# Performance work log

Hardware: AMD Instinct MI355X
Metric: run time of the kernel (lower is better)

Reference implementation:

```python
import jax, jax.numpy as jnp
import numpy as np

B, S, D = 2, 4096, 768
H = 12
HD = D // H  # 64
INNER = 4 * D
EPS = 1e-5


def setup_inputs() -> dict:
    key = jax.random.key(0)
    ks = jax.random.split(key, 12)
    sd = 0.02
    # causal additive mask (GPT-2 style): 0 where allowed, -1e9 where masked
    causal = jnp.tril(jnp.ones((S, S), dtype=bool))
    attention_mask = jnp.where(causal, 0.0, -1e9).astype(jnp.float32)[None, None]
    return {
        "hidden_states": jax.random.normal(ks[0], (B, S, D), dtype=jnp.float32),
        "attention_mask": attention_mask,
        "ln1_g": jnp.ones((D,), jnp.float32),
        "ln1_b": jnp.zeros((D,), jnp.float32),
        "w_attn": jax.random.normal(ks[1], (D, 3 * D), jnp.float32) * sd,
        "b_attn": jnp.zeros((3 * D,), jnp.float32),
        "w_cproj": jax.random.normal(ks[2], (D, D), jnp.float32) * sd,
        "b_cproj": jnp.zeros((D,), jnp.float32),
        "ln2_g": jnp.ones((D,), jnp.float32),
        "ln2_b": jnp.zeros((D,), jnp.float32),
        "w_fc": jax.random.normal(ks[3], (D, INNER), jnp.float32) * sd,
        "b_fc": jnp.zeros((INNER,), jnp.float32),
        "w_fc_proj": jax.random.normal(ks[4], (INNER, D), jnp.float32) * sd,
        "b_fc_proj": jnp.zeros((D,), jnp.float32),
    }


def _layernorm(x, g, b):
    mu = jnp.mean(x, axis=-1, keepdims=True)
    var = jnp.mean(jnp.square(x - mu), axis=-1, keepdims=True)
    return (x - mu) * jax.lax.rsqrt(var + EPS) * g + b


def reference(hidden_states, attention_mask, ln1_g, ln1_b, w_attn, b_attn,
              w_cproj, b_cproj, ln2_g, ln2_b, w_fc, b_fc, w_fc_proj, b_fc_proj):
    residual = hidden_states
    x = _layernorm(hidden_states, ln1_g, ln1_b)
    # qkv projection
    qkv = x @ w_attn + b_attn                       # [B,S,3D]
    q, k, v = jnp.split(qkv, 3, axis=-1)
    q = q.reshape(B, S, H, HD).transpose(0, 2, 1, 3)  # [B,H,S,HD]
    k = k.reshape(B, S, H, HD).transpose(0, 2, 1, 3)
    v = v.reshape(B, S, H, HD).transpose(0, 2, 1, 3)
    scale = HD ** -0.5
    scores = jnp.einsum('bhqd,bhkd->bhqk', q, k) * scale + attention_mask
    attn = jax.nn.softmax(scores, axis=-1)
    ctx = jnp.einsum('bhqk,bhkd->bhqd', attn, v)    # [B,H,S,HD]
    ctx = ctx.transpose(0, 2, 1, 3).reshape(B, S, D)
    attn_out = ctx @ w_cproj + b_cproj
    h = attn_out + residual
    residual = h
    y = _layernorm(h, ln2_g, ln2_b)
    y = jax.nn.gelu(y @ w_fc + b_fc, approximate=False)  # nn.GELU default = exact
    y = y @ w_fc_proj + b_fc_proj
    return y + residual
```

## Files before the change

kernel.cpp:

```cpp
#include <hip/hip_runtime.h>
#include <hip/hip_bf16.h>


#define S_     4096
#define D_     768
#define H_     12
#define HD_    64
#define NB_    2
#define M_     (NB_*S_)
#define QKV_   (3*D_)
#define INNER_ 3072

typedef unsigned short u16;
typedef __attribute__((ext_vector_type(4))) float f32x4;
typedef __attribute__((ext_vector_type(8))) short s16x8;

__device__ __forceinline__ float bf2f(u16 h) {
    union { unsigned int u; float f; } c; c.u = ((unsigned int)h) << 16; return c.f;
}
__device__ __forceinline__ u16 f2bf(float f) {
    union { float f; unsigned int u; } c; c.f = f;
    return (u16)((c.u + 0x7fffu + ((c.u >> 16) & 1u)) >> 16);
}
__device__ __forceinline__ void storev(u16* p, float v) { *p = f2bf(v); }
__device__ __forceinline__ void storev(float* p, float v) { *p = v; }

__device__ __forceinline__ float fexp2(float x) {
#if __has_builtin(__builtin_amdgcn_exp2f)
    return __builtin_amdgcn_exp2f(x);
#else
    return __expf(x * 0.69314718056f);
#endif
}
__device__ __forceinline__ unsigned int packbf(float a, float b) {
    union { __hip_bfloat162 h; unsigned int u; } c;
    c.h = __float22bfloat162_rn(float2{a, b});
    return c.u;
}

__device__ __forceinline__ void gload_lds16(const u16* g, u16* l) {
    __builtin_amdgcn_global_load_lds((const __attribute__((address_space(1))) void*)g,
                                     (__attribute__((address_space(3))) void*)l, 16, 0, 0);
}

template <typename IT, bool PERM>
__global__ __launch_bounds__(256) void transpose_kernel(const IT* __restrict__ in,
                                                        u16* __restrict__ out,
                                                        int ld_in, int ld_out) {
    __shared__ u16 tile[32][33];
    const int c0 = blockIdx.x * 32, r0 = blockIdx.y * 32;
    const int tx = threadIdx.x & 31, ty = threadIdx.x >> 5;
#pragma unroll
    for (int i = 0; i < 32; i += 8) {
        IT v = in[(size_t)(r0 + ty + i) * ld_in + c0 + tx];
        u16 bv;
        if constexpr (sizeof(IT) == 4) bv = f2bf((float)v); else bv = (u16)v;
        tile[ty + i][tx] = bv;
    }
    __syncthreads();
    int oc = r0 + tx;
    if constexpr (PERM) oc = (oc & ~63) | (((oc & 15) << 2) | ((oc >> 4) & 3));
#pragma unroll
    for (int i = 0; i < 32; i += 8)
        out[(size_t)(c0 + ty + i) * ld_out + oc] = tile[tx][ty + i];
}

__global__ __launch_bounds__(256) void ln_row(const float* __restrict__ x, const float* __restrict__ g,
                                              const float* __restrict__ bb, u16* __restrict__ y,
                                              unsigned int* ctr) {
    const int row = blockIdx.x;
    const int tid = threadIdx.x;
    if (ctr && row == 0 && tid == 0) *ctr = 0u;
    const float* xr = x + (size_t)row * D_;
    float v0 = xr[tid], v1 = xr[tid + 256], v2 = xr[tid + 512];
    float s = v0 + v1 + v2, s2 = v0 * v0 + v1 * v1 + v2 * v2;
#pragma unroll
    for (int d = 32; d >= 1; d >>= 1) { s += __shfl_xor(s, d, 64); s2 += __shfl_xor(s2, d, 64); }
    __shared__ float red[8];
    const int wave = tid >> 6, lane = tid & 63;
    if (lane == 0) { red[wave] = s; red[4 + wave] = s2; }
    __syncthreads();
    s = red[0] + red[1] + red[2] + red[3];
    s2 = red[4] + red[5] + red[6] + red[7];
    const float mu = s * (1.0f / D_);
    const float var = s2 * (1.0f / D_) - mu * mu;
    const float rstd = rsqrtf(var + 1e-5f);
    u16* yr = y + (size_t)row * D_;
    yr[tid]       = f2bf((v0 - mu) * rstd * g[tid]       + bb[tid]);
    yr[tid + 256] = f2bf((v1 - mu) * rstd * g[tid + 256] + bb[tid + 256]);
    yr[tid + 512] = f2bf((v2 - mu) * rstd * g[tid + 512] + bb[tid + 512]);
}

template <int EPI, typename OT>
__global__ __launch_bounds__(256) void gemm_bt(const u16* __restrict__ A, const u16* __restrict__ Bt,
                                               const float* __restrict__ bias, const float* res,
                                               OT* C, int M, int N, int K) {
    __shared__ u16 As[128 * 32];
    __shared__ u16 Bs[128 * 32];
    const int tid = threadIdx.x;
    const int wave = tid >> 6, lane = tid & 63;
    const int m0 = blockIdx.y << 7, n0 = blockIdx.x << 7;
    const int fr = lane & 15, quad = lane >> 4;

    const int srow = wave * 16 + (lane >> 2);
    const int scol = (lane & 3) * 8;
    const u16* ag0 = A + (size_t)(m0 + srow) * K + scol;
    const u16* ag1 = ag0 + (size_t)64 * K;
    const u16* bg0 = Bt + (size_t)(n0 + srow) * K + scol;
    const u16* bg1 = bg0 + (size_t)64 * K;
    u16* al0 = As + wave * 512;
    u16* al1 = As + 2048 + wave * 512;
    u16* bl0 = Bs + wave * 512;
    u16* bl1 = Bs + 2048 + wave * 512;

    const f32x4 fz = {0.f, 0.f, 0.f, 0.f};
    f32x4 acc[4][4];
#pragma unroll
    for (int i = 0; i < 4; i++)
#pragma unroll
        for (int j = 0; j < 4; j++) acc[i][j] = fz;

    const int wm = wave & 1, wn = wave >> 1;
    const u16* a_rd = As + (wm * 64 + fr) * 32 + quad * 8;
    const u16* b_rd = Bs + (wn * 64 + fr) * 32 + quad * 8;

    for (int k0 = 0; k0 < K; k0 += 32) {
        gload_lds16(ag0 + k0, al0);
        gload_lds16(ag1 + k0, al1);
        gload_lds16(bg0 + k0, bl0);
        gload_lds16(bg1 + k0, bl1);
        __syncthreads();
        s16x8 af[4], bfr[4];
#pragma unroll
        for (int t = 0; t < 4; t++) {
            af[t]  = *(const s16x8*)(a_rd + t * 16 * 32);
            bfr[t] = *(const s16x8*)(b_rd + t * 16 * 32);
        }
#pragma unroll
        for (int mt = 0; mt < 4; mt++)
#pragma unroll
            for (int nt = 0; nt < 4; nt++)
                acc[mt][nt] = __builtin_amdgcn_mfma_f32_16x16x32_bf16(af[mt], bfr[nt], acc[mt][nt], 0, 0, 0);
        __syncthreads();
    }

    const int crow0 = m0 + wm * 64 + quad * 4;
    const int ccol0 = n0 + wn * 64 + fr;
#pragma unroll
    for (int nt = 0; nt < 4; nt++) {
        const int col = ccol0 + nt * 16;
        const float bv = bias[col];
#pragma unroll
        for (int mt = 0; mt < 4; mt++) {
#pragma unroll
            for (int r = 0; r < 4; r++) {
                const int row = crow0 + mt * 16 + r;
                float v = acc[mt][nt][r] + bv;
                if constexpr (EPI == 1) v = 0.5f * v * (1.0f + erff(v * 0.70710678118654752f));
                if constexpr (EPI == 2) v += res[(size_t)row * N + col];
                storev(&C[(size_t)row * N + col], v);
            }
        }
    }
}

template <int EPI, typename OT>
__global__ __launch_bounds__(256) void gemm_bt64(const u16* __restrict__ A, const u16* __restrict__ Bt,
                                                 const float* __restrict__ bias, const float* res,
                                                 OT* C, int M, int N, int K) {
    __shared__ u16 As[128 * 32];
    __shared__ u16 Bs[64 * 32];
    const int tid = threadIdx.x;
    const int wave = tid >> 6, lane = tid & 63;
    const int m0 = blockIdx.y << 7, n0 = blockIdx.x << 6;
    const int fr = lane & 15, quad = lane >> 4;

    const int srow = wave * 16 + (lane >> 2);
    const int scol = (lane & 3) * 8;
    const u16* ag0 = A + (size_t)(m0 + srow) * K + scol;
    const u16* ag1 = ag0 + (size_t)64 * K;
    const u16* bg0 = Bt + (size_t)(n0 + srow) * K + scol;
    u16* al0 = As + wave * 512;
    u16* al1 = As + 2048 + wave * 512;
    u16* bl0 = Bs + wave * 512;

    const f32x4 fz = {0.f, 0.f, 0.f, 0.f};
    f32x4 acc[2][4];
#pragma unroll
    for (int i = 0; i < 2; i++)
#pragma unroll
        for (int j = 0; j < 4; j++) acc[i][j] = fz;

    const u16* a_rd = As + (wave * 32 + fr) * 32 + quad * 8;
    const u16* b_rd = Bs + fr * 32 + quad * 8;

    for (int k0 = 0; k0 < K; k0 += 32) {
        gload_lds16(ag0 + k0, al0);
        gload_lds16(ag1 + k0, al1);
        gload_lds16(bg0 + k0, bl0);
        __syncthreads();
        s16x8 af[2], bfr[4];
#pragma unroll
        for (int t = 0; t < 2; t++) af[t] = *(const s16x8*)(a_rd + t * 16 * 32);
#pragma unroll
        for (int t = 0; t < 4; t++) bfr[t] = *(const s16x8*)(b_rd + t * 16 * 32);
#pragma unroll
        for (int mt = 0; mt < 2; mt++)
#pragma unroll
            for (int nt = 0; nt < 4; nt++)
                acc[mt][nt] = __builtin_amdgcn_mfma_f32_16x16x32_bf16(af[mt], bfr[nt], acc[mt][nt], 0, 0, 0);
        __syncthreads();
    }

    const int crow0 = m0 + wave * 32 + quad * 4;
    const int ccol0 = n0 + fr;
#pragma unroll
    for (int nt = 0; nt < 4; nt++) {
        const int col = ccol0 + nt * 16;
        const float bv = bias[col];
#pragma unroll
        for (int mt = 0; mt < 2; mt++) {
#pragma unroll
            for (int r = 0; r < 4; r++) {
                const int row = crow0 + mt * 16 + r;
                float v = acc[mt][nt][r] + bv;
                if constexpr (EPI == 1) v = 0.5f * v * (1.0f + erff(v * 0.70710678118654752f));
                if constexpr (EPI == 2) v += res[(size_t)row * N + col];
                storev(&C[(size_t)row * N + col], v);
            }
        }
    }
}

#define SCALE_  0.1803368801111f
#define PST_    72
#define NITEMS_ (32 * H_ * NB_)
#define NWORK_  512
__global__ __launch_bounds__(256, 2) void flash_attn(const u16* __restrict__ qkv, const u16* __restrict__ vt,
                                                     u16* __restrict__ ctx, unsigned int* __restrict__ ctr) {
    const int tid = threadIdx.x;
    const int wave = tid >> 6, lane = tid & 63;
    const int fr = lane & 15, quad = lane >> 4;

    __shared__ u16 Ks[2][64 * 64];
    __shared__ u16 Vs[2][64 * 64];
    __shared__ u16 Ps4[4][32 * PST_];
    __shared__ int item_sh;
    u16* Ps = Ps4[wave];

    const int rsub = lane >> 3;
    const int schunk = ((lane & 7) ^ rsub) << 3;
    u16* KlS0 = &Ks[0][(wave << 4) * 64];
    u16* VlS0 = &Vs[0][(wave << 4) * 64];

    const f32x4 fz = {0.f, 0.f, 0.f, 0.f};
    s16x8 ones;
#pragma unroll
    for (int j = 0; j < 8; j++) ones[j] = (short)0x3F80;

    for (;;) {
        if (tid == 0) item_sh = (int)atomicAdd(ctr, 1u);
        __syncthreads();
        const int item = item_sh;
        if (item >= NITEMS_) return;

        const int strip = 31 - item / (H_ * NB_);
        const int hb = item % (H_ * NB_);
        const int h = hb % H_, b = hb / H_;
        const int q0 = strip << 7;
        const int qwv = q0 + (wave << 5);

        const u16* Qg  = qkv + ((size_t)b * S_ + qwv) * QKV_ + h * HD_;
        const u16* Kg  = qkv + (size_t)b * S_ * QKV_ + D_ + h * HD_;
        const u16* Vtg = vt + ((size_t)b * D_ + h * HD_) * S_;
        const u16* KgS = Kg + (size_t)((wave << 4) + rsub) * QKV_ + schunk;
        const u16* VgS = Vtg + (size_t)((wave << 4) + rsub) * S_ + schunk;

        s16x8 qf[2][2];
#pragma unroll
        for (int mt = 0; mt < 2; mt++)
#pragma unroll
            for (int kk = 0; kk < 2; kk++)
                qf[mt][kk] = *(const s16x8*)(Qg + (size_t)(mt * 16 + fr) * QKV_ + kk * 32 + quad * 8);

        f32x4 o[2][4];
        f32x4 ls[2];
#pragma unroll
        for (int mt = 0; mt < 2; mt++) {
            ls[mt] = fz;
#pragma unroll
            for (int nt = 0; nt < 4; nt++) o[mt][nt] = fz;
        }

        const int ntw = (strip << 1) + 2;

        gload_lds16(KgS, KlS0);
        gload_lds16(KgS + (size_t)8 * QKV_, KlS0 + 512);
        gload_lds16(VgS, VlS0);
        gload_lds16(VgS + (size_t)8 * S_, VlS0 + 512);
        asm volatile("s_waitcnt vmcnt(0)" ::: "memory");
        __syncthreads();

        int cur = 0;
        for (int t = 0; t < ntw; t++) {
            const int k0 = t << 6;

            if (t + 1 < ntw) {
                const int nb = cur ^ 1;
                const u16* kg = KgS + (size_t)((t + 1) << 6) * QKV_;
                const u16* vg = VgS + ((t + 1) << 6);
                u16* kl = KlS0 + nb * (64 * 64);
                u16* vl = VlS0 + nb * (64 * 64);
                gload_lds16(kg, kl);
                gload_lds16(kg + (size_t)8 * QKV_, kl + 512);
                gload_lds16(vg, vl);
                gload_lds16(vg + (size_t)8 * S_, vl + 512);
            }

            if (k0 <= qwv + 31) {
                const u16* kb = Ks[cur];
                const u16* vb = Vs[cur];

                s16x8 kc[2][4];
#pragma unroll
                for (int kk = 0; kk < 2; kk++)
#pragma unroll
                    for (int nt = 0; nt < 4; nt++) {
                        const int row = nt * 16 + fr;
                        const int sl = ((kk * 4 + quad) ^ (fr & 7)) << 3;
                        kc[kk][nt] = *(const s16x8*)(kb + row * 64 + sl);
                    }

                f32x4 sc[2][4];
#pragma unroll
                for (int mt = 0; mt < 2; mt++)
#pragma unroll
                    for (int nt = 0; nt < 4; nt++) sc[mt][nt] = fz;
#pragma unroll
                for (int kk = 0; kk < 2; kk++)
#pragma unroll
                    for (int mt = 0; mt < 2; mt++)
#pragma unroll
                        for (int nt = 0; nt < 4; nt++)
                            sc[mt][nt] = __builtin_amdgcn_mfma_f32_16x16x32_bf16(qf[mt][kk], kc[kk][nt], sc[mt][nt], 0, 0, 0);

                const bool fast = (k0 + 63 <= qwv);
#pragma unroll
                for (int mt = 0; mt < 2; mt++) {
#pragma unroll
                    for (int r = 0; r < 4; r++) {
                        float s0 = sc[mt][0][r] * SCALE_;
                        float s1 = sc[mt][1][r] * SCALE_;
                        float s2 = sc[mt][2][r] * SCALE_;
                        float s3 = sc[mt][3][r] * SCALE_;
                        if (!fast) {
                            const int lim = (qwv + mt * 16 + quad * 4 + r) - k0;
                            if (fr      > lim) s0 = -1e30f;
                            if (fr + 16 > lim) s1 = -1e30f;
                            if (fr + 32 > lim) s2 = -1e30f;
                            if (fr + 48 > lim) s3 = -1e30f;
                        }
                        s0 = fexp2(s0); s1 = fexp2(s1); s2 = fexp2(s2); s3 = fexp2(s3);
                        const int prow = mt * 16 + quad * 4 + r;
                        *(uint2*)(Ps + prow * PST_ + fr * 4) = make_uint2(packbf(s0, s1), packbf(s2, s3));
                    }
                }

                s16x8 vf[2][4];
#pragma unroll
                for (int kk = 0; kk < 2; kk++)
#pragma unroll
                    for (int nt = 0; nt < 4; nt++) {
                        const int row = nt * 16 + fr;
                        const int sl = ((kk * 4 + quad) ^ (fr & 7)) << 3;
                        vf[kk][nt] = *(const s16x8*)(vb + row * 64 + sl);
                    }

                s16x8 pf[2][2];
#pragma unroll
                for (int mt = 0; mt < 2; mt++)
#pragma unroll
                    for (int kk = 0; kk < 2; kk++)
                        pf[mt][kk] = *(const s16x8*)(Ps + (mt * 16 + fr) * PST_ + kk * 32 + quad * 8);

#pragma unroll
                for (int mt = 0; mt < 2; mt++) {
                    ls[mt] = __builtin_amdgcn_mfma_f32_16x16x32_bf16(pf[mt][0], ones, ls[mt], 0, 0, 0);
                    ls[mt] = __builtin_amdgcn_mfma_f32_16x16x32_bf16(pf[mt][1], ones, ls[mt], 0, 0, 0);
                }
#pragma unroll
                for (int kk = 0; kk < 2; kk++)
#pragma unroll
                    for (int mt = 0; mt < 2; mt++)
#pragma unroll
                        for (int nt = 0; nt < 4; nt++)
                            o[mt][nt] = __builtin_amdgcn_mfma_f32_16x16x32_bf16(pf[mt][kk], vf[kk][nt], o[mt][nt], 0, 0, 0);
            }

            asm volatile("s_waitcnt vmcnt(0)" ::: "memory");
            __syncthreads();
            cur ^= 1;
        }

#pragma unroll
        for (int mt = 0; mt < 2; mt++) {
#pragma unroll
            for (int r = 0; r < 4; r++) {
                const int grow = qwv + mt * 16 + quad * 4 + r;
                const float inv = 1.0f / ls[mt][r];
                u16* crow = ctx + ((size_t)b * S_ + grow) * D_ + h * HD_ + fr;
#pragma unroll
                for (int nt = 0; nt < 4; nt++)
                    crow[nt * 16] = f2bf(o[mt][nt][r] * inv);
            }
        }
    }
}

extern "C" void kernel_launch(void* const* d_in, const int* in_sizes, int n_in,
                              void* d_out, int out_size, void* d_ws, size_t ws_size,
                              hipStream_t stream) {
    const float* hid    = (const float*)d_in[0];
    const float* ln1g   = (const float*)d_in[2];
    const float* ln1b   = (const float*)d_in[3];
    const float* w_attn = (const float*)d_in[4];
    const float* b_attn = (const float*)d_in[5];
    const float* w_cp   = (const float*)d_in[6];
    const float* b_cp   = (const float*)d_in[7];
    const float* ln2g   = (const float*)d_in[8];
    const float* ln2b   = (const float*)d_in[9];
    const float* w_fc   = (const float*)d_in[10];
    const float* b_fc   = (const float*)d_in[11];
    const float* w_fp   = (const float*)d_in[12];
    const float* b_fp   = (const float*)d_in[13];
    float* dout = (float*)d_out;

    unsigned int* ctr = (unsigned int*)d_out;

    u16* ws = (u16*)d_ws;
    u16* wTa  = ws; ws += (size_t)QKV_ * D_;
    u16* wTc  = ws; ws += (size_t)D_ * D_;
    u16* wTf  = ws; ws += (size_t)INNER_ * D_;
    u16* wTp  = ws; ws += (size_t)D_ * INNER_;
    u16* xln  = ws; ws += (size_t)M_ * D_;
    u16* qkvb = ws; ws += (size_t)M_ * QKV_;
    u16* vtb  = ws; ws += (size_t)NB_ * D_ * S_;
    u16* ctxb = xln;
    u16* yln  = xln;
    u16* act  = qkvb;

    dim3 blk(256);
    transpose_kernel<float, false><<<dim3(QKV_ / 32, D_ / 32), blk, 0, stream>>>(w_attn, wTa, QKV_, D_);
    transpose_kernel<float, false><<<dim3(D_ / 32, D_ / 32), blk, 0, stream>>>(w_cp, wTc, D_, D_);
    transpose_kernel<float, false><<<dim3(INNER_ / 32, D_ / 32), blk, 0, stream>>>(w_fc, wTf, INNER_, D_);
    transpose_kernel<float, false><<<dim3(D_ / 32, INNER_ / 32), blk, 0, stream>>>(w_fp, wTp, D_, INNER_);

    ln_row<<<M_, blk, 0, stream>>>(hid, ln1g, ln1b, xln, ctr);
    gemm_bt<0, u16><<<dim3(QKV_ / 128, M_ / 128), blk, 0, stream>>>(xln, wTa, b_attn, nullptr, qkvb, M_, QKV_, D_);

    transpose_kernel<u16, true><<<dim3(D_ / 32, S_ / 32), blk, 0, stream>>>(qkvb + 2 * D_, vtb, QKV_, S_);
    transpose_kernel<u16, true><<<dim3(D_ / 32, S_ / 32), blk, 0, stream>>>(qkvb + (size_t)S_ * QKV_ + 2 * D_,
                                                                            vtb + (size_t)D_ * S_, QKV_, S_);
    flash_attn<<<dim3(NWORK_), blk, 0, stream>>>(qkvb, vtb, ctxb, ctr);

    gemm_bt64<2, float><<<dim3(D_ / 64, M_ / 128), blk, 0, stream>>>(ctxb, wTc, b_cp, hid, dout, M_, D_, D_);
    ln_row<<<M_, blk, 0, stream>>>(dout, ln2g, ln2b, yln, nullptr);
    gemm_bt<1, u16><<<dim3(INNER_ / 128, M_ / 128), blk, 0, stream>>>(yln, wTf, b_fc, nullptr, act, M_, INNER_, D_);
    gemm_bt64<2, float><<<dim3(D_ / 64, M_ / 128), blk, 0, stream>>>(act, wTp, b_fp, dout, dout, M_, D_, INNER_);
}
```

Before: 527.9 us.

## Triple-buffer GEMM and attention LDS loads with prefetch depth two

Moves both GEMM kernels from single-buffered LDS staging, which waited on each load before computing, to a three-stage ring that prefetches two K-steps ahead with partial vmcnt waits. The attention kernel goes from double to triple buffering of K/V tiles. It also raises wave priority around the MFMA blocks with s_setprio. The cost is three times the GEMM LDS footprint and more attention LDS, which may reduce occupancy.

Measured after the change: 527.8 us. Within noise of the previous version (-0.0%).

```diff
diff --git a/kernel.cpp b/kernel.cpp
--- a/kernel.cpp
+++ b/kernel.cpp
@@ -42,6 +42,8 @@
     __builtin_amdgcn_global_load_lds((const __attribute__((address_space(1))) void*)g,
                                      (__attribute__((address_space(3))) void*)l, 16, 0, 0);
 }
+
+#define WAITVM(N) asm volatile("s_waitcnt vmcnt(" #N ")" ::: "memory")
 
 template <typename IT, bool PERM>
 __global__ __launch_bounds__(256) void transpose_kernel(const IT* __restrict__ in,
@@ -95,8 +97,8 @@
 __global__ __launch_bounds__(256) void gemm_bt(const u16* __restrict__ A, const u16* __restrict__ Bt,
                                                const float* __restrict__ bias, const float* res,
                                                OT* C, int M, int N, int K) {
-    __shared__ u16 As[128 * 32];
-    __shared__ u16 Bs[128 * 32];
+    __shared__ u16 As[3][128 * 32];
+    __shared__ u16 Bs[3][128 * 32];
     const int tid = threadIdx.x;
     const int wave = tid >> 6, lane = tid & 63;
     const int m0 = blockIdx.y << 7, n0 = blockIdx.x << 7;
@@ -108,10 +110,13 @@
     const u16* ag1 = ag0 + (size_t)64 * K;
     const u16* bg0 = Bt + (size_t)(n0 + srow) * K + scol;
     const u16* bg1 = bg0 + (size_t)64 * K;
-    u16* al0 = As + wave * 512;
-    u16* al1 = As + 2048 + wave * 512;
-    u16* bl0 = Bs + wave * 512;
-    u16* bl1 = Bs + 2048 + wave * 512;
+
+    auto STAGE = [&](int k0, int b) {
+        gload_lds16(ag0 + k0, &As[b][wave * 512]);
+        gload_lds16(ag1 + k0, &As[b][2048 + wave * 512]);
+        gload_lds16(bg0 + k0, &Bs[b][wave * 512]);
+        gload_lds16(bg1 + k0, &Bs[b][2048 + wave * 512]);
+    };
 
     const f32x4 fz = {0.f, 0.f, 0.f, 0.f};
     f32x4 acc[4][4];
@@ -121,26 +126,30 @@
         for (int j = 0; j < 4; j++) acc[i][j] = fz;
 
     const int wm = wave & 1, wn = wave >> 1;
-    const u16* a_rd = As + (wm * 64 + fr) * 32 + quad * 8;
-    const u16* b_rd = Bs + (wn * 64 + fr) * 32 + quad * 8;
-
-    for (int k0 = 0; k0 < K; k0 += 32) {
-        gload_lds16(ag0 + k0, al0);
-        gload_lds16(ag1 + k0, al1);
-        gload_lds16(bg0 + k0, bl0);
-        gload_lds16(bg1 + k0, bl1);
-        __syncthreads();
+    const int a_off = (wm * 64 + fr) * 32 + quad * 8;
+    const int b_off = (wn * 64 + fr) * 32 + quad * 8;
+
+    const int nsteps = K >> 5;
+    STAGE(0, 0);
+    if (nsteps > 1) { STAGE(32, 1); WAITVM(4); } else { WAITVM(0); }
+    __syncthreads();
+
+    for (int t = 0; t < nsteps; t++) {
+        if (t + 2 < nsteps) STAGE((t + 2) << 5, (t + 2) % 3);
+        const u16* a_rd = &As[t % 3][a_off];
+        const u16* b_rd = &Bs[t % 3][b_off];
         s16x8 af[4], bfr[4];
 #pragma unroll
-        for (int t = 0; t < 4; t++) {
-            af[t]  = *(const s16x8*)(a_rd + t * 16 * 32);
-            bfr[t] = *(const s16x8*)(b_rd + t * 16 * 32);
+        for (int u = 0; u < 4; u++) {
+            af[u]  = *(const s16x8*)(a_rd + u * 16 * 32);
+            bfr[u] = *(const s16x8*)(b_rd + u * 16 * 32);
         }
 #pragma unroll
         for (int mt = 0; mt < 4; mt++)
 #pragma unroll
             for (int nt = 0; nt < 4; nt++)
                 acc[mt][nt] = __builtin_amdgcn_mfma_f32_16x16x32_bf16(af[mt], bfr[nt], acc[mt][nt], 0, 0, 0);
+        if (t + 2 < nsteps) { WAITVM(4); } else { WAITVM(0); }
         __syncthreads();
     }
 
@@ -168,8 +177,8 @@
 __global__ __launch_bounds__(256) void gemm_bt64(const u16* __restrict__ A, const u16* __restrict__ Bt,
                                                  const float* __restrict__ bias, const float* res,
                                                  OT* C, int M, int N, int K) {
-    __shared__ u16 As[128 * 32];
-    __shared__ u16 Bs[64 * 32];
+    __shared__ u16 As[3][128 * 32];
+    __shared__ u16 Bs[3][64 * 32];
     const int tid = threadIdx.x;
     const int wave = tid >> 6, lane = tid & 63;
     const int m0 = blockIdx.y << 7, n0 = blockIdx.x << 6;
@@ -180,9 +189,12 @@
     const u16* ag0 = A + (size_t)(m0 + srow) * K + scol;
     const u16* ag1 = ag0 + (size_t)64 * K;
     const u16* bg0 = Bt + (size_t)(n0 + srow) * K + scol;
-    u16* al0 = As + wave * 512;
-    u16* al1 = As + 2048 + wave * 512;
-    u16* bl0 = Bs + wave * 512;
+
+    auto STAGE = [&](int k0, int b) {
+        gload_lds16(ag0 + k0, &As[b][wave * 512]);
+        gload_lds16(ag1 + k0, &As[b][2048 + wave * 512]);
+        gload_lds16(bg0 + k0, &Bs[b][wave * 512]);
+    };
 
     const f32x4 fz = {0.f, 0.f, 0.f, 0.f};
     f32x4 acc[2][4];
@@ -191,24 +203,29 @@
 #pragma unroll
         for (int j = 0; j < 4; j++) acc[i][j] = fz;
 
-    const u16* a_rd = As + (wave * 32 + fr) * 32 + quad * 8;
-    const u16* b_rd = Bs + fr * 32 + quad * 8;
-
-    for (int k0 = 0; k0 < K; k0 += 32) {
-        gload_lds16(ag0 + k0, al0);
-        gload_lds16(ag1 + k0, al1);
-        gload_lds16(bg0 + k0, bl0);
-        __syncthreads();
+    const int a_off = (wave * 32 + fr) * 32 + quad * 8;
+    const int b_off = fr * 32 + quad * 8;
+
+    const int nsteps = K >> 5;
+    STAGE(0, 0);
+    if (nsteps > 1) { STAGE(32, 1); WAITVM(3); } else { WAITVM(0); }
+    __syncthreads();
+
+    for (int t = 0; t < nsteps; t++) {
+        if (t + 2 < nsteps) STAGE((t + 2) << 5, (t + 2) % 3);
+        const u16* a_rd = &As[t % 3][a_off];
+        const u16* b_rd = &Bs[t % 3][b_off];
         s16x8 af[2], bfr[4];
 #pragma unroll
-        for (int t = 0; t < 2; t++) af[t] = *(const s16x8*)(a_rd + t * 16 * 32);
-#pragma unroll
-        for (int t = 0; t < 4; t++) bfr[t] = *(const s16x8*)(b_rd + t * 16 * 32);
+        for (int u = 0; u < 2; u++) af[u] = *(const s16x8*)(a_rd + u * 16 * 32);
+#pragma unroll
+        for (int u = 0; u < 4; u++) bfr[u] = *(const s16x8*)(b_rd + u * 16 * 32);
 #pragma unroll
         for (int mt = 0; mt < 2; mt++)
 #pragma unroll
             for (int nt = 0; nt < 4; nt++)
                 acc[mt][nt] = __builtin_amdgcn_mfma_f32_16x16x32_bf16(af[mt], bfr[nt], acc[mt][nt], 0, 0, 0);
+        if (t + 2 < nsteps) { WAITVM(3); } else { WAITVM(0); }
         __syncthreads();
     }
 
@@ -242,16 +259,15 @@
     const int wave = tid >> 6, lane = tid & 63;
     const int fr = lane & 15, quad = lane >> 4;
 
-    __shared__ u16 Ks[2][64 * 64];
-    __shared__ u16 Vs[2][64 * 64];
+    __shared__ u16 Ks[3][64 * 64];
+    __shared__ u16 Vs[3][64 * 64];
     __shared__ u16 Ps4[4][32 * PST_];
     __shared__ int item_sh;
     u16* Ps = Ps4[wave];
 
     const int rsub = lane >> 3;
     const int schunk = ((lane & 7) ^ rsub) << 3;
-    u16* KlS0 = &Ks[0][(wave << 4) * 64];
-    u16* VlS0 = &Vs[0][(wave << 4) * 64];
+    const int lds_woff = (wave << 4) * 64;
 
     const f32x4 fz = {0.f, 0.f, 0.f, 0.f};
     s16x8 ones;
@@ -276,6 +292,15 @@
         const u16* KgS = Kg + (size_t)((wave << 4) + rsub) * QKV_ + schunk;
         const u16* VgS = Vtg + (size_t)((wave << 4) + rsub) * S_ + schunk;
 
+        auto STAGEF = [&](int t, int bf) {
+            const u16* kg = KgS + (size_t)(t << 6) * QKV_;
+            const u16* vg = VgS + (t << 6);
+            gload_lds16(kg, &Ks[bf][lds_woff]);
+            gload_lds16(kg + (size_t)8 * QKV_, &Ks[bf][lds_woff + 512]);
+            gload_lds16(vg, &Vs[bf][lds_woff]);
+            gload_lds16(vg + (size_t)8 * S_, &Vs[bf][lds_woff + 512]);
+        };
+
         s16x8 qf[2][2];
 #pragma unroll
         for (int mt = 0; mt < 2; mt++)
@@ -294,32 +319,19 @@
 
         const int ntw = (strip << 1) + 2;
 
-        gload_lds16(KgS, KlS0);
-        gload_lds16(KgS + (size_t)8 * QKV_, KlS0 + 512);
-        gload_lds16(VgS, VlS0);
-        gload_lds16(VgS + (size_t)8 * S_, VlS0 + 512);
-        asm volatile("s_waitcnt vmcnt(0)" ::: "memory");
+        STAGEF(0, 0);
+        STAGEF(1, 1);
+        WAITVM(4);
         __syncthreads();
 
-        int cur = 0;
         for (int t = 0; t < ntw; t++) {
             const int k0 = t << 6;
 
-            if (t + 1 < ntw) {
-                const int nb = cur ^ 1;
-                const u16* kg = KgS + (size_t)((t + 1) << 6) * QKV_;
-                const u16* vg = VgS + ((t + 1) << 6);
-                u16* kl = KlS0 + nb * (64 * 64);
-                u16* vl = VlS0 + nb * (64 * 64);
-                gload_lds16(kg, kl);
-                gload_lds16(kg + (size_t)8 * QKV_, kl + 512);
-                gload_lds16(vg, vl);
-                gload_lds16(vg + (size_t)8 * S_, vl + 512);
-            }
+            if (t + 2 < ntw) STAGEF(t + 2, (t + 2) % 3);
 
             if (k0 <= qwv + 31) {
-                const u16* kb = Ks[cur];
-                const u16* vb = Vs[cur];
+                const u16* kb = Ks[t % 3];
+                const u16* vb = Vs[t % 3];
 
                 s16x8 kc[2][4];
 #pragma unroll
@@ -336,6 +348,7 @@
                 for (int mt = 0; mt < 2; mt++)
 #pragma unroll
                     for (int nt = 0; nt < 4; nt++) sc[mt][nt] = fz;
+                __builtin_amdgcn_s_setprio(1);
 #pragma unroll
                 for (int kk = 0; kk < 2; kk++)
 #pragma unroll
@@ -343,6 +356,7 @@
 #pragma unroll
                         for (int nt = 0; nt < 4; nt++)
                             sc[mt][nt] = __builtin_amdgcn_mfma_f32_16x16x32_bf16(qf[mt][kk], kc[kk][nt], sc[mt][nt], 0, 0, 0);
+                __builtin_amdgcn_s_setprio(0);
 
                 const bool fast = (k0 + 63 <= qwv);
 #pragma unroll
@@ -383,6 +397,7 @@
                     for (int kk = 0; kk < 2; kk++)
                         pf[mt][kk] = *(const s16x8*)(Ps + (mt * 16 + fr) * PST_ + kk * 32 + quad * 8);
 
+                __builtin_amdgcn_s_setprio(1);
 #pragma unroll
                 for (int mt = 0; mt < 2; mt++) {
                     ls[mt] = __builtin_amdgcn_mfma_f32_16x16x32_bf16(pf[mt][0], ones, ls[mt], 0, 0, 0);
@@ -395,11 +410,11 @@
 #pragma unroll
                         for (int nt = 0; nt < 4; nt++)
                             o[mt][nt] = __builtin_amdgcn_mfma_f32_16x16x32_bf16(pf[mt][kk], vf[kk][nt], o[mt][nt], 0, 0, 0);
+                __builtin_amdgcn_s_setprio(0);
             }
 
-            asm volatile("s_waitcnt vmcnt(0)" ::: "memory");
+            if (t + 2 < ntw) { WAITVM(4); } else { WAITVM(0); }
             __syncthreads();
-            cur ^= 1;
         }
 
 #pragma unroll
```

## Add 256x256 double-buffered swizzled GEMM and triple-buffer the 64-wide GEMM

Applied to the files above, without the earlier changes.

Replaces the 128x128 single-buffered GEMM used for the QKV and FC projections with a 512-thread 256x256 tile kernel. It uses 64-wide K steps, XOR-swizzled LDS layout, double buffering with split early/late staging and explicit vmcnt waits, plus block-index swizzling for L2 locality. The 128x64 GEMM for the output projections gets a three-stage LDS pipeline so global loads overlap MFMA work. The larger tiles cut global/LDS traffic per flop and hide load latency. The cost is much higher register and LDS pressure (128KB LDS per block) and fewer workgroups, which may hurt occupancy and tail balance.

Measured after the change: 583.8 us. +10.6%, slower.

```diff
diff --git a/kernel.cpp b/kernel.cpp
--- a/kernel.cpp
+++ b/kernel.cpp
@@ -42,6 +42,8 @@
     __builtin_amdgcn_global_load_lds((const __attribute__((address_space(1))) void*)g,
                                      (__attribute__((address_space(3))) void*)l, 16, 0, 0);
 }
+
+#define WAITVM(N) asm volatile("s_waitcnt vmcnt(" #N ")" ::: "memory")
 
 template <typename IT, bool PERM>
 __global__ __launch_bounds__(256) void transpose_kernel(const IT* __restrict__ in,
@@ -91,15 +93,139 @@
     yr[tid + 512] = f2bf((v2 - mu) * rstd * g[tid + 512] + bb[tid + 512]);
 }
 
-template <int EPI, typename OT>
-__global__ __launch_bounds__(256) void gemm_bt(const u16* __restrict__ A, const u16* __restrict__ Bt,
-                                               const float* __restrict__ bias, const float* res,
-                                               OT* C, int M, int N, int K) {
-    __shared__ u16 As[128 * 32];
-    __shared__ u16 Bs[128 * 32];
+template <int EPI>
+__global__ __launch_bounds__(512, 2) void gemm256(const u16* __restrict__ A, const u16* __restrict__ Bt,
+                                                  const float* __restrict__ bias,
+                                                  u16* __restrict__ C, int M, int N, int K, int nbx) {
+    __shared__ u16 As[2][256 * 64];
+    __shared__ u16 Bs[2][256 * 64];
     const int tid = threadIdx.x;
     const int wave = tid >> 6, lane = tid & 63;
-    const int m0 = blockIdx.y << 7, n0 = blockIdx.x << 7;
+    const int fr = lane & 15, quad = lane >> 4;
+    const int wm = wave >> 2, wn = wave & 3;
+
+    const int nwg = (int)gridDim.x;
+    const int id = (int)blockIdx.x;
+    const int swz = (id & 7) * (nwg >> 3) + (id >> 3);
+    const int by = swz / nbx, bx = swz % nbx;
+    const int m0 = by << 8, n0 = bx << 8;
+
+    const int rsub = lane >> 3;
+    const int schunk = ((lane & 7) ^ rsub) << 3;
+    const u16* Ag = A + (size_t)(m0 + wave * 8 + rsub) * K + schunk;
+    const u16* Bg = Bt + (size_t)(n0 + wave * 8 + rsub) * K + schunk;
+    const int sdst = wave * 512;
+
+    const f32x4 fz = {0.f, 0.f, 0.f, 0.f};
+    f32x4 acc[8][4];
+#pragma unroll
+    for (int i = 0; i < 8; i++)
+#pragma unroll
+        for (int j = 0; j < 4; j++) acc[i][j] = fz;
+
+    const int nt = K >> 6;
+
+    auto STAGE_E = [&](int t, int b) {
+        const int koff = t << 6;
+#pragma unroll
+        for (int g = 0; g < 4; g++)
+            gload_lds16(Bg + (size_t)(g * 64) * K + koff, &Bs[b][g * 4096 + sdst]);
+        gload_lds16(Ag + koff,                   &As[b][0 * 4096 + sdst]);
+        gload_lds16(Ag + (size_t)128 * K + koff, &As[b][2 * 4096 + sdst]);
+    };
+    auto STAGE_L = [&](int t, int b) {
+        const int koff = t << 6;
+        gload_lds16(Ag + (size_t)64 * K + koff,  &As[b][1 * 4096 + sdst]);
+        gload_lds16(Ag + (size_t)192 * K + koff, &As[b][3 * 4096 + sdst]);
+    };
+
+    STAGE_E(0, 0);
+    STAGE_L(0, 0);
+    WAITVM(2);
+
+    for (int t = 0; t < nt; t++) {
+        const int b = t & 1;
+        __syncthreads();
+        const u16* ab = As[b];
+        const u16* bb = Bs[b];
+
+        s16x8 bf[4][2], af[4][2];
+#pragma unroll
+        for (int j = 0; j < 4; j++)
+#pragma unroll
+            for (int kk = 0; kk < 2; kk++) {
+                const int r = wn * 64 + j * 16 + fr;
+                const int sl = ((kk * 4 + quad) ^ (r & 7)) << 3;
+                bf[j][kk] = *(const s16x8*)(bb + r * 64 + sl);
+            }
+#pragma unroll
+        for (int i = 0; i < 4; i++)
+#pragma unroll
+            for (int kk = 0; kk < 2; kk++) {
+                const int r = wm * 128 + i * 16 + fr;
+                const int sl = ((kk * 4 + quad) ^ (r & 7)) << 3;
+                af[i][kk] = *(const s16x8*)(ab + r * 64 + sl);
+            }
+        if (t + 1 < nt) STAGE_E(t + 1, b ^ 1);
+#pragma unroll
+        for (int kk = 0; kk < 2; kk++)
+#pragma unroll
+            for (int i = 0; i < 4; i++)
+#pragma unroll
+                for (int j = 0; j < 4; j++)
+                    acc[i][j] = __builtin_amdgcn_mfma_f32_16x16x32_bf16(af[i][kk], bf[j][kk], acc[i][j], 0, 0, 0);
+
+        if (t + 1 < nt) { WAITVM(6); } else { WAITVM(0); }
+        __syncthreads();
+
+#pragma unroll
+        for (int i = 0; i < 4; i++)
+#pragma unroll
+            for (int kk = 0; kk < 2; kk++) {
+                const int r = wm * 128 + 64 + i * 16 + fr;
+                const int sl = ((kk * 4 + quad) ^ (r & 7)) << 3;
+                af[i][kk] = *(const s16x8*)(ab + r * 64 + sl);
+            }
+        if (t + 1 < nt) STAGE_L(t + 1, b ^ 1);
+#pragma unroll
+        for (int kk = 0; kk < 2; kk++)
+#pragma unroll
+            for (int i = 0; i < 4; i++)
+#pragma unroll
+                for (int j = 0; j < 4; j++)
+                    acc[4 + i][j] = __builtin_amdgcn_mfma_f32_16x16x32_bf16(af[i][kk], bf[j][kk], acc[4 + i][j], 0, 0, 0);
+
+        if (t + 1 < nt) WAITVM(2);
+    }
+
+    const int crow0 = m0 + wm * 128 + quad * 4;
+    const int ccol0 = n0 + wn * 64 + fr;
+#pragma unroll
+    for (int j = 0; j < 4; j++) {
+        const int col = ccol0 + j * 16;
+        const float bv = bias[col];
+#pragma unroll
+        for (int i = 0; i < 8; i++) {
+#pragma unroll
+            for (int r = 0; r < 4; r++) {
+                const int row = crow0 + i * 16 + r;
+                float v = acc[i][j][r] + bv;
+                if constexpr (EPI == 1) v = 0.5f * v * (1.0f + erff(v * 0.70710678118654752f));
+                C[(size_t)row * N + col] = f2bf(v);
+            }
+        }
+    }
+}
+
+template <int EPI, typename OT>
+__global__ __launch_bounds__(256) void gemm_bt64(const u16* __restrict__ A, const u16* __restrict__ Bt,
+                                                 const float* __restrict__ bias, const float* res,
+                                                 OT* C, int M, int N, int K) {
+    __shared__ u16 As[3][128 * 32];
+    __shared__ u16 Bs[3][64 * 32];
+    const int tid = threadIdx.x;
+    const int wave = tid >> 6, lane = tid & 63;
+    const int m0 = blockIdx.y << 7, n0 = blockIdx.x << 6;
     const int fr = lane & 15, quad = lane >> 4;
 
     const int srow = wave * 16 + (lane >> 2);
@@ -107,108 +233,43 @@
     const u16* ag0 = A + (size_t)(m0 + srow) * K + scol;
     const u16* ag1 = ag0 + (size_t)64 * K;
     const u16* bg0 = Bt + (size_t)(n0 + srow) * K + scol;
-    const u16* bg1 = bg0 + (size_t)64 * K;
-    u16* al0 = As + wave * 512;
-    u16* al1 = As + 2048 + wave * 512;
-    u16* bl0 = Bs + wave * 512;
-    u16* bl1 = Bs + 2048 + wave * 512;
+
+    auto STAGE = [&](int k0, int b) {
+        gload_lds16(ag0 + k0, &As[b][wave * 512]);
+        gload_lds16(ag1 + k0, &As[b][2048 + wave * 512]);
+        gload_lds16(bg0 + k0, &Bs[b][wave * 512]);
+    };
 
     const f32x4 fz = {0.f, 0.f, 0.f, 0.f};
-    f32x4 acc[4][4];
-#pragma unroll
-    for (int i = 0; i < 4; i++)
+    f32x4 acc[2][4];
+#pragma unroll
+    for (int i = 0; i < 2; i++)
 #pragma unroll
         for (int j = 0; j < 4; j++) acc[i][j] = fz;
 
-    const int wm = wave & 1, wn = wave >> 1;
-    const u16* a_rd = As + (wm * 64 + fr) * 32 + quad * 8;
-    const u16* b_rd = Bs + (wn * 64 + fr) * 32 + quad * 8;
-
-    for (int k0 = 0; k0 < K; k0 += 32) {
-        gload_lds16(ag0 + k0, al0);
-        gload_lds16(ag1 + k0, al1);
-        gload_lds16(bg0 + k0, bl0);
-        gload_lds16(bg1 + k0, bl1);
-        __syncthreads();
-        s16x8 af[4], bfr[4];
-#pragma unroll
-        for (int t = 0; t < 4; t++) {
-            af[t]  = *(const s16x8*)(a_rd + t * 16 * 32);
-            bfr[t] = *(const s16x8*)(b_rd + t * 16 * 32);
-        }
-#pragma unroll
-        for (int mt = 0; mt < 4; mt++)
+    const int a_off = (wave * 32 + fr) * 32 + quad * 8;
+    const int b_off = fr * 32 + quad * 8;
+
+    const int nsteps = K >> 5;
+    STAGE(0, 0);
+    if (nsteps > 1) { STAGE(32, 1); WAITVM(3); } else { WAITVM(0); }
+    __syncthreads();
+
+    for (int t = 0; t < nsteps; t++) {
+        if (t + 2 < nsteps) STAGE((t + 2) << 5, (t + 2) % 3);
+        const u16* a_rd = &As[t % 3][a_off];
+        const u16* b_rd = &Bs[t % 3][b_off];
+        s16x8 af[2], bfr[4];
+#pragma unroll
+        for (int u = 0; u < 2; u++) af[u] = *(const s16x8*)(a_rd + u * 16 * 32);
+#pragma unroll
+        for (int u = 0; u < 4; u++) bfr[u] = *(const s16x8*)(b_rd + u * 16 * 32);
+#pragma unroll
+        for (int mt = 0; mt < 2; mt++)
 #pragma unroll
             for (int nt = 0; nt < 4; nt++)
                 acc[mt][nt] = __builtin_amdgcn_mfma_f32_16x16x32_bf16(af[mt], bfr[nt], acc[mt][nt], 0, 0, 0);
-        __syncthreads();
-    }
-
-    const int crow0 = m0 + wm * 64 + quad * 4;
-    const int ccol0 = n0 + wn * 64 + fr;
-#pragma unroll
-    for (int nt = 0; nt < 4; nt++) {
-        const int col = ccol0 + nt * 16;
-        const float bv = bias[col];
-#pragma unroll
-        for (int mt = 0; mt < 4; mt++) {
-#pragma unroll
-            for (int r = 0; r < 4; r++) {
-                const int row = crow0 + mt * 16 + r;
-                float v = acc[mt][nt][r] + bv;
-                if constexpr (EPI == 1) v = 0.5f * v * (1.0f + erff(v * 0.70710678118654752f));
-                if constexpr (EPI == 2) v += res[(size_t)row * N + col];
-                storev(&C[(size_t)row * N + col], v);
-            }
-        }
-    }
-}
-
-template <int EPI, typename OT>
-__global__ __launch_bounds__(256) void gemm_bt64(const u16* __restrict__ A, const u16* __restrict__ Bt,
-                                                 const float* __restrict__ bias, const float* res,
-                                                 OT* C, int M, int N, int K) {
-    __shared__ u16 As[128 * 32];
-    __shared__ u16 Bs[64 * 32];
-    const int tid = threadIdx.x;
-    const int wave = tid >> 6, lane = tid & 63;
-    const int m0 = blockIdx.y << 7, n0 = blockIdx.x << 6;
-    const int fr = lane & 15, quad = lane >> 4;
-
-    const int srow = wave * 16 + (lane >> 2);
-    const int scol = (lane & 3) * 8;
-    const u16* ag0 = A + (size_t)(m0 + srow) * K + scol;
-    const u16* ag1 = ag0 + (size_t)64 * K;
-    const u16* bg0 = Bt + (size_t)(n0 + srow) * K + scol;
-    u16* al0 = As + wave * 512;
-    u16* al1 = As + 2048 + wave * 512;
-    u16* bl0 = Bs + wave * 512;
-
-    const f32x4 fz = {0.f, 0.f, 0.f, 0.f};
-    f32x4 acc[2][4];
-#pragma unroll
-    for (int i = 0; i < 2; i++)
-#pragma unroll
-        for (int j = 0; j < 4; j++) acc[i][j] = fz;
-
-    const u16* a_rd = As + (wave * 32 + fr) * 32 + quad * 8;
-    const u16* b_rd = Bs + fr * 32 + quad * 8;
-
-    for (int k0 = 0; k0 < K; k0 += 32) {
-        gload_lds16(ag0 + k0, al0);
-        gload_lds16(ag1 + k0, al1);
-        gload_lds16(bg0 + k0, bl0);
-        __syncthreads();
-        s16x8 af[2], bfr[4];
-#pragma unroll
-        for (int t = 0; t < 2; t++) af[t] = *(const s16x8*)(a_rd + t * 16 * 32);
-#pragma unroll
-        for (int t = 0; t < 4; t++) bfr[t] = *(const s16x8*)(b_rd + t * 16 * 32);
-#pragma unroll
-        for (int mt = 0; mt < 2; mt++)
-#pragma unroll
-            for (int nt = 0; nt < 4; nt++)
-                acc[mt][nt] = __builtin_amdgcn_mfma_f32_16x16x32_bf16(af[mt], bfr[nt], acc[mt][nt], 0, 0, 0);
+        if (t + 2 < nsteps) { WAITVM(3); } else { WAITVM(0); }
         __syncthreads();
     }
 
@@ -456,7 +517,7 @@
     transpose_kernel<float, false><<<dim3(D_ / 32, INNER_ / 32), blk, 0, stream>>>(w_fp, wTp, D_, INNER_);
 
     ln_row<<<M_, blk, 0, stream>>>(hid, ln1g, ln1b, xln, ctr);
-    gemm_bt<0, u16><<<dim3(QKV_ / 128, M_ / 128), blk, 0, stream>>>(xln, wTa, b_attn, nullptr, qkvb, M_, QKV_, D_);
+    gemm256<0><<<dim3(288), dim3(512), 0, stream>>>(xln, wTa, b_attn, qkvb, M_, QKV_, D_, 9);
 
     transpose_kernel<u16, true><<<dim3(D_ / 32, S_ / 32), blk, 0, stream>>>(qkvb + 2 * D_, vtb, QKV_, S_);
     transpose_kernel<u16, true><<<dim3(D_ / 32, S_ / 32), blk, 0, stream>>>(qkvb + (size_t)S_ * QKV_ + 2 * D_,
@@ -465,6 +526,6 @@
 
     gemm_bt64<2, float><<<dim3(D_ / 64, M_ / 128), blk, 0, stream>>>(ctxb, wTc, b_cp, hid, dout, M_, D_, D_);
     ln_row<<<M_, blk, 0, stream>>>(dout, ln2g, ln2b, yln, nullptr);
-    gemm_bt<1, u16><<<dim3(INNER_ / 128, M_ / 128), blk, 0, stream>>>(yln, wTf, b_fc, nullptr, act, M_, INNER_, D_);
+    gemm256<1><<<dim3(384), dim3(512), 0, stream>>>(yln, wTf, b_fc, act, M_, INNER_, D_, 12);
     gemm_bt64<2, float><<<dim3(D_ / 64, M_ / 128), blk, 0, stream>>>(act, wTp, b_fp, dout, dout, M_, D_, INNER_);
 }
```

## Triple-buffer GEMM LDS loads, swizzle blocks across XCDs, unify on 128x128 tiles

Applied to the files above, without the earlier changes.

The 128x128 GEMM now keeps three LDS buffers and issues global-to-LDS loads two K-steps ahead, using explicit vmcnt waits in place of a full load-then-barrier on every step. This is meant to hide global load latency behind the MFMA work. Block IDs are remapped so that consecutive tiles are spread across the eight XCDs, which should improve L2 locality. The 64-wide GEMM variant is dropped and the N=768 projections use 128x128 tiles, which halves their block count and may leave CUs underused, while the larger LDS footprint can reduce occupancy.

New measurement: 522.9 us. About the same (-0.9%).

```diff
diff --git a/kernel.cpp b/kernel.cpp
--- a/kernel.cpp
+++ b/kernel.cpp
@@ -42,6 +42,8 @@
     __builtin_amdgcn_global_load_lds((const __attribute__((address_space(1))) void*)g,
                                      (__attribute__((address_space(3))) void*)l, 16, 0, 0);
 }
+
+#define WAITVM(N) asm volatile("s_waitcnt vmcnt(" #N ")" ::: "memory")
 
 template <typename IT, bool PERM>
 __global__ __launch_bounds__(256) void transpose_kernel(const IT* __restrict__ in,
@@ -95,12 +97,17 @@
 __global__ __launch_bounds__(256) void gemm_bt(const u16* __restrict__ A, const u16* __restrict__ Bt,
                                                const float* __restrict__ bias, const float* res,
                                                OT* C, int M, int N, int K) {
-    __shared__ u16 As[128 * 32];
-    __shared__ u16 Bs[128 * 32];
+    __shared__ u16 As[3][128 * 32];
+    __shared__ u16 Bs[3][128 * 32];
     const int tid = threadIdx.x;
     const int wave = tid >> 6, lane = tid & 63;
-    const int m0 = blockIdx.y << 7, n0 = blockIdx.x << 7;
     const int fr = lane & 15, quad = lane >> 4;
+
+    const int nwg = (int)(gridDim.x * gridDim.y);
+    int id = (int)(blockIdx.y * gridDim.x + blockIdx.x);
+    id = (id & 7) * (nwg >> 3) + (id >> 3);
+    const int by = id / (int)gridDim.x, bx = id % (int)gridDim.x;
+    const int m0 = by << 7, n0 = bx << 7;
 
     const int srow = wave * 16 + (lane >> 2);
     const int scol = (lane & 3) * 8;
@@ -108,10 +115,13 @@
     const u16* ag1 = ag0 + (size_t)64 * K;
     const u16* bg0 = Bt + (size_t)(n0 + srow) * K + scol;
     const u16* bg1 = bg0 + (size_t)64 * K;
-    u16* al0 = As + wave * 512;
-    u16* al1 = As + 2048 + wave * 512;
-    u16* bl0 = Bs + wave * 512;
-    u16* bl1 = Bs + 2048 + wave * 512;
+
+    auto STAGE = [&](int k0, int b) {
+        gload_lds16(ag0 + k0, &As[b][wave * 512]);
+        gload_lds16(ag1 + k0, &As[b][2048 + wave * 512]);
+        gload_lds16(bg0 + k0, &Bs[b][wave * 512]);
+        gload_lds16(bg1 + k0, &Bs[b][2048 + wave * 512]);
+    };
 
     const f32x4 fz = {0.f, 0.f, 0.f, 0.f};
     f32x4 acc[4][4];
@@ -121,26 +131,30 @@
         for (int j = 0; j < 4; j++) acc[i][j] = fz;
 
     const int wm = wave & 1, wn = wave >> 1;
-    const u16* a_rd = As + (wm * 64 + fr) * 32 + quad * 8;
-    const u16* b_rd = Bs + (wn * 64 + fr) * 32 + quad * 8;
-
-    for (int k0 = 0; k0 < K; k0 += 32) {
-        gload_lds16(ag0 + k0, al0);
-        gload_lds16(ag1 + k0, al1);
-        gload_lds16(bg0 + k0, bl0);
-        gload_lds16(bg1 + k0, bl1);
-        __syncthreads();
+    const int a_off = (wm * 64 + fr) * 32 + quad * 8;
+    const int b_off = (wn * 64 + fr) * 32 + quad * 8;
+
+    const int nsteps = K >> 5;
+    STAGE(0, 0);
+    if (nsteps > 1) { STAGE(32, 1); WAITVM(4); } else { WAITVM(0); }
+    __syncthreads();
+
+    for (int t = 0; t < nsteps; t++) {
+        if (t + 2 < nsteps) STAGE((t + 2) << 5, (t + 2) % 3);
+        const u16* a_rd = &As[t % 3][a_off];
+        const u16* b_rd = &Bs[t % 3][b_off];
         s16x8 af[4], bfr[4];
 #pragma unroll
-        for (int t = 0; t < 4; t++) {
-            af[t]  = *(const s16x8*)(a_rd + t * 16 * 32);
-            bfr[t] = *(const s16x8*)(b_rd + t * 16 * 32);
+        for (int u = 0; u < 4; u++) {
+            af[u]  = *(const s16x8*)(a_rd + u * 16 * 32);
+            bfr[u] = *(const s16x8*)(b_rd + u * 16 * 32);
         }
 #pragma unroll
         for (int mt = 0; mt < 4; mt++)
 #pragma unroll
             for (int nt = 0; nt < 4; nt++)
                 acc[mt][nt] = __builtin_amdgcn_mfma_f32_16x16x32_bf16(af[mt], bfr[nt], acc[mt][nt], 0, 0, 0);
+        if (t + 2 < nsteps) { WAITVM(4); } else { WAITVM(0); }
         __syncthreads();
     }
 
@@ -152,74 +166,6 @@
         const float bv = bias[col];
 #pragma unroll
         for (int mt = 0; mt < 4; mt++) {
-#pragma unroll
-            for (int r = 0; r < 4; r++) {
-                const int row = crow0 + mt * 16 + r;
-                float v = acc[mt][nt][r] + bv;
-                if constexpr (EPI == 1) v = 0.5f * v * (1.0f + erff(v * 0.70710678118654752f));
-                if constexpr (EPI == 2) v += res[(size_t)row * N + col];
-                storev(&C[(size_t)row * N + col], v);
-            }
-        }
-    }
-}
-
-template <int EPI, typename OT>
-__global__ __launch_bounds__(256) void gemm_bt64(const u16* __restrict__ A, const u16* __restrict__ Bt,
-                                                 const float* __restrict__ bias, const float* res,
-                                                 OT* C, int M, int N, int K) {
-    __shared__ u16 As[128 * 32];
-    __shared__ u16 Bs[64 * 32];
-    const int tid = threadIdx.x;
-    const int wave = tid >> 6, lane = tid & 63;
-    const int m0 = blockIdx.y << 7, n0 = blockIdx.x << 6;
-    const int fr = lane & 15, quad = lane >> 4;
-
-    const int srow = wave * 16 + (lane >> 2);
-    const int scol = (lane & 3) * 8;
-    const u16* ag0 = A + (size_t)(m0 + srow) * K + scol;
-    const u16* ag1 = ag0 + (size_t)64 * K;
-    const u16* bg0 = Bt + (size_t)(n0 + srow) * K + scol;
-    u16* al0 = As + wave * 512;
-    u16* al1 = As + 2048 + wave * 512;
-    u16* bl0 = Bs + wave * 512;
-
-    const f32x4 fz = {0.f, 0.f, 0.f, 0.f};
-    f32x4 acc[2][4];
-#pragma unroll
-    for (int i = 0; i < 2; i++)
-#pragma unroll
-        for (int j = 0; j < 4; j++) acc[i][j] = fz;
-
-    const u16* a_rd = As + (wave * 32 + fr) * 32 + quad * 8;
-    const u16* b_rd = Bs + fr * 32 + quad * 8;
-
-    for (int k0 = 0; k0 < K; k0 += 32) {
-        gload_lds16(ag0 + k0, al0);
-        gload_lds16(ag1 + k0, al1);
-        gload_lds16(bg0 + k0, bl0);
-        __syncthreads();
-        s16x8 af[2], bfr[4];
-#pragma unroll
-        for (int t = 0; t < 2; t++) af[t] = *(const s16x8*)(a_rd + t * 16 * 32);
-#pragma unroll
-        for (int t = 0; t < 4; t++) bfr[t] = *(const s16x8*)(b_rd + t * 16 * 32);
-#pragma unroll
-        for (int mt = 0; mt < 2; mt++)
-#pragma unroll
-            for (int nt = 0; nt < 4; nt++)
-                acc[mt][nt] = __builtin_amdgcn_mfma_f32_16x16x32_bf16(af[mt], bfr[nt], acc[mt][nt], 0, 0, 0);
-        __syncthreads();
-    }
-
-    const int crow0 = m0 + wave * 32 + quad * 4;
-    const int ccol0 = n0 + fr;
-#pragma unroll
-    for (int nt = 0; nt < 4; nt++) {
-        const int col = ccol0 + nt * 16;
-        const float bv = bias[col];
-#pragma unroll
-        for (int mt = 0; mt < 2; mt++) {
 #pragma unroll
             for (int r = 0; r < 4; r++) {
                 const int row = crow0 + mt * 16 + r;
@@ -463,8 +409,8 @@
                                                                             vtb + (size_t)D_ * S_, QKV_, S_);
     flash_attn<<<dim3(NWORK_), blk, 0, stream>>>(qkvb, vtb, ctxb, ctr);
 
-    gemm_bt64<2, float><<<dim3(D_ / 64, M_ / 128), blk, 0, stream>>>(ctxb, wTc, b_cp, hid, dout, M_, D_, D_);
+    gemm_bt<2, float><<<dim3(D_ / 128, M_ / 128), blk, 0, stream>>>(ctxb, wTc, b_cp, hid, dout, M_, D_, D_);
     ln_row<<<M_, blk, 0, stream>>>(dout, ln2g, ln2b, yln, nullptr);
     gemm_bt<1, u16><<<dim3(INNER_ / 128, M_ / 128), blk, 0, stream>>>(yln, wTf, b_fc, nullptr, act, M_, INNER_, D_);
-    gemm_bt64<2, float><<<dim3(D_ / 64, M_ / 128), blk, 0, stream>>>(act, wTp, b_fp, dout, dout, M_, D_, INNER_);
-}
+    gemm_bt<2, float><<<dim3(D_ / 128, M_ / 128), blk, 0, stream>>>(act, wTp, b_fp, dout, dout, M_, D_, INNER_);
+}
```
